# Kernel optimization log

Measured on AMD Instinct MI355X. Metric: run time of the kernel, lower is better.

The kernel has to match this reference:

```python
import jax, jax.numpy as jnp
import numpy as np

SQ, SK, B, H, D = 2048, 2048, 2, 16, 64
LAYER_NUMBER = 1  # coeff for query_key_layer_scaling
MASK_FILL = -10000.0  # attention_mask_func fill value


def setup_inputs() -> dict:
    key = jax.random.key(0)
    kq, kk, kv = jax.random.split(key, 3)
    query_layer = jax.random.normal(kq, (SQ, B, H, D), dtype=jnp.float32)
    key_layer = jax.random.normal(kk, (SK, B, H, D), dtype=jnp.float32)
    value_layer = jax.random.normal(kv, (SK, B, H, D), dtype=jnp.float32)
    attention_mask = jnp.zeros((B, 1, SQ, SK), dtype=bool)  # ignored for causal mask type
    return {
        "query_layer": query_layer,
        "key_layer": key_layer,
        "value_layer": value_layer,
        "attention_mask": attention_mask,
    }


def reference(query_layer, key_layer, value_layer, attention_mask):
    sq, b, h, d = query_layer.shape
    sk = key_layer.shape[0]
    coeff = float(LAYER_NUMBER)
    norm_factor = np.sqrt(d) * coeff  # norm_factor = sqrt(d) * layer_number

    # BMM1: [b,h,sq,sk] scores, scaled by 1/norm_factor
    scores = jnp.einsum("sbhd,tbhd->bhst", query_layer, key_layer) / norm_factor

    # FusedScaleMaskSoftmax: scale by coeff in fp32, causal mask, softmax
    scores = scores.astype(jnp.float32) * coeff
    causal = jnp.triu(jnp.ones((sq, sk), dtype=bool), k=1)  # True above diagonal -> masked
    scores = jnp.where(causal[None, None], MASK_FILL, scores)
    probs = jax.nn.softmax(scores, axis=-1).astype(query_layer.dtype)

    # dropout p=0.0 -> identity

    # BMM2: context [sq,b,h,d] -> [sq,b,h*d]
    context = jnp.einsum("bhst,tbhd->sbhd", probs, value_layer)
    return context.reshape(sq, b, h * d)
```

## Files before the change

kernel.cpp:

```cpp
#include <hip/hip_runtime.h>

typedef short bf16x8 __attribute__((ext_vector_type(8)));
typedef float f32x4 __attribute__((ext_vector_type(4)));
typedef unsigned u32x4 __attribute__((ext_vector_type(4)));
typedef unsigned u32x2 __attribute__((ext_vector_type(2)));
typedef unsigned short ushort_t;

#define RS 2048
#define LDSK 72
#define QSCALE 0.18033688011f
#define BH_STRIDE (2048*64)

static __device__ __forceinline__ unsigned pkbf(float a, float b) {
    union { float f; unsigned u; } ua, ub; ua.f = a; ub.f = b;
    return ((ua.u + 0x8000u) >> 16) | ((ub.u + 0x8000u) & 0xffff0000u);
}

static __device__ __forceinline__ float fexp2(float x) {
#if __has_builtin(__builtin_amdgcn_exp2f)
    return __builtin_amdgcn_exp2f(x);
#else
    return exp2f(x);
#endif
}

__global__ __launch_bounds__(256)
void prep_bf16(const float* __restrict__ K, const float* __restrict__ V,
               ushort_t* __restrict__ Kbf, ushort_t* __restrict__ Vtb)
{
    __shared__ short Tt[64 * LDSK];
    const int kt = blockIdx.x, bh = blockIdx.y;
    const int t = threadIdx.x;

    {
        const int key = t >> 2, cq = (t & 3) * 16;
        const float* kp = K + (size_t)(kt * 64 + key) * RS + bh * 64 + cq;
        f32x4 a0 = *(const f32x4*)kp,     a1 = *(const f32x4*)(kp + 4);
        f32x4 a2 = *(const f32x4*)(kp + 8), a3 = *(const f32x4*)(kp + 12);
        u32x4 w0, w1;
        w0[0] = pkbf(a0[0], a0[1]); w0[1] = pkbf(a0[2], a0[3]);
        w0[2] = pkbf(a1[0], a1[1]); w0[3] = pkbf(a1[2], a1[3]);
        w1[0] = pkbf(a2[0], a2[1]); w1[1] = pkbf(a2[2], a2[3]);
        w1[2] = pkbf(a3[0], a3[1]); w1[3] = pkbf(a3[2], a3[3]);
        ushort_t* kout = Kbf + (size_t)bh * BH_STRIDE + (size_t)(kt * 64 + key) * 64 + cq;
        *(u32x4*)kout = w0;
        *(u32x4*)(kout + 8) = w1;
    }
    {
        const int vkey = (t & 31) * 2, vd = (t >> 5) * 8;
        const float* vp = V + (size_t)(kt * 64 + vkey) * RS + bh * 64 + vd;
        f32x4 b0 = *(const f32x4*)vp,        b1 = *(const f32x4*)(vp + 4);
        f32x4 c0 = *(const f32x4*)(vp + RS), c1 = *(const f32x4*)(vp + RS + 4);
        #pragma unroll
        for (int i = 0; i < 4; ++i) {
            *(unsigned*)&Tt[(vd + i) * LDSK + vkey]     = pkbf(b0[i], c0[i]);
            *(unsigned*)&Tt[(vd + 4 + i) * LDSK + vkey] = pkbf(b1[i], c1[i]);
        }
    }
    __syncthreads();
    {
        const int d = t >> 2, kq = (t & 3) * 16;
        ushort_t* vout = Vtb + (size_t)bh * BH_STRIDE + (size_t)d * RS + kt * 64 + kq;
        u32x4 w0 = *(const u32x4*)&Tt[d * LDSK + kq];
        u32x4 w1 = *(const u32x4*)&Tt[d * LDSK + kq + 8];
        *(u32x4*)vout = w0;
        *(u32x4*)(vout + 8) = w1;
    }
}

__global__ __launch_bounds__(256, 4)
void fa_fwd2(const float* __restrict__ Q, const ushort_t* __restrict__ Kbf,
             const ushort_t* __restrict__ Vtb, float* __restrict__ Out)
{
    __shared__ short Ksh[64 * LDSK];
    __shared__ short Vt[64 * LDSK];
    __shared__ short Psh[4][16 * LDSK];

    const int x = blockIdx.x;
    const int chunk = x >> 8, idx = x & 255;
    const int bh = idx & 31, s = idx >> 5;
    const int qt = (chunk == 0) ? (31 - s) : (chunk == 1) ? (23 - s)
                 : (chunk == 2) ? s : (8 + s);
    const int base = bh * 64;
    const int tid = threadIdx.x;
    const int wave = tid >> 6, lane = tid & 63;
    const int n15 = lane & 15, quad = lane >> 4;
    const int q0 = qt * 64;

    const int r0 = tid >> 3, cc = (tid & 7) * 8;
    const ushort_t* kb = Kbf + (size_t)bh * BH_STRIDE + r0 * 64 + cc;
    const ushort_t* vb = Vtb + (size_t)bh * BH_STRIDE + (size_t)r0 * RS + cc;

    bf16x8 qf[2];
    {
        const float* qp = Q + (size_t)(q0 + wave * 16 + n15) * RS + base + quad * 8;
        #pragma unroll
        for (int ks = 0; ks < 2; ++ks) {
            f32x4 a0 = *(const f32x4*)(qp + ks * 32) * QSCALE;
            f32x4 a1 = *(const f32x4*)(qp + ks * 32 + 4) * QSCALE;
            union { u32x4 u; bf16x8 s; } w;
            w.u[0] = pkbf(a0[0], a0[1]); w.u[1] = pkbf(a0[2], a0[3]);
            w.u[2] = pkbf(a1[0], a1[1]); w.u[3] = pkbf(a1[2], a1[3]);
            qf[ks] = w.s;
        }
    }

    f32x4 O[4];
    #pragma unroll
    for (int i = 0; i < 4; ++i) O[i] = (f32x4){0.f, 0.f, 0.f, 0.f};
    float l = 0.f;

    u32x4 pk0, pk1, pv0, pv1;
    auto prefetch = [&](int kt) {
        const ushort_t* kp = kb + (size_t)kt * 4096;
        pk0 = *(const u32x4*)kp;
        pk1 = *(const u32x4*)(kp + 32 * 64);
        const ushort_t* vp = vb + kt * 64;
        pv0 = *(const u32x4*)vp;
        pv1 = *(const u32x4*)(vp + 32 * RS);
    };
    auto stage = [&]() {
        *(u32x4*)&Ksh[r0 * LDSK + cc] = pk0;
        *(u32x4*)&Ksh[(r0 + 32) * LDSK + cc] = pk1;
        *(u32x4*)&Vt[r0 * LDSK + cc] = pv0;
        *(u32x4*)&Vt[(r0 + 32) * LDSK + cc] = pv1;
    };

    auto compute = [&](int kb_, bool diag) {
        f32x4 S[4];
        #pragma unroll
        for (int mb = 0; mb < 4; ++mb) {
            f32x4 sv = (f32x4){0.f, 0.f, 0.f, 0.f};
            bf16x8 kf0 = *(const bf16x8*)&Ksh[(mb * 16 + n15) * LDSK + quad * 8];
            sv = __builtin_amdgcn_mfma_f32_16x16x32_bf16(kf0, qf[0], sv, 0, 0, 0);
            bf16x8 kf1 = *(const bf16x8*)&Ksh[(mb * 16 + n15) * LDSK + 32 + quad * 8];
            sv = __builtin_amdgcn_mfma_f32_16x16x32_bf16(kf1, qf[1], sv, 0, 0, 0);
            S[mb] = sv;
        }
        if (diag) {
            int q = q0 + wave * 16 + n15;
            #pragma unroll
            for (int mb = 0; mb < 4; ++mb)
                #pragma unroll
                for (int r = 0; r < 4; ++r)
                    if (kb_ + mb * 16 + quad * 4 + r > q) S[mb][r] = -1e30f;
        }
        float rs = 0.f;
        #pragma unroll
        for (int mb = 0; mb < 4; ++mb) {
            float p0 = fexp2(S[mb][0]), p1 = fexp2(S[mb][1]);
            float p2 = fexp2(S[mb][2]), p3 = fexp2(S[mb][3]);
            rs += (p0 + p1) + (p2 + p3);
            u32x2 w; w[0] = pkbf(p0, p1); w[1] = pkbf(p2, p3);
            *(u32x2*)&Psh[wave][n15 * LDSK + mb * 16 + quad * 4] = w;
        }
        rs += __shfl_xor(rs, 16);
        rs += __shfl_xor(rs, 32);
        l += rs;
        bf16x8 pf0 = *(const bf16x8*)&Psh[wave][n15 * LDSK + quad * 8];
        bf16x8 pf1 = *(const bf16x8*)&Psh[wave][n15 * LDSK + 32 + quad * 8];
        #pragma unroll
        for (int db = 0; db < 4; ++db) {
            bf16x8 vf0 = *(const bf16x8*)&Vt[(db * 16 + n15) * LDSK + quad * 8];
            O[db] = __builtin_amdgcn_mfma_f32_16x16x32_bf16(pf0, vf0, O[db], 0, 0, 0);
            bf16x8 vf1 = *(const bf16x8*)&Vt[(db * 16 + n15) * LDSK + 32 + quad * 8];
            O[db] = __builtin_amdgcn_mfma_f32_16x16x32_bf16(pf1, vf1, O[db], 0, 0, 0);
        }
    };

    prefetch(0);
    for (int kt = 0; kt <= qt; ++kt) {
        __syncthreads();
        stage();
        __syncthreads();
        if (kt < qt) prefetch(kt + 1);
        compute(kt * 64, kt == qt);
    }

    #pragma unroll
    for (int r = 0; r < 4; ++r) {
        float inv = 1.0f / __shfl(l, quad * 4 + r);
        size_t row = (size_t)(q0 + wave * 16 + quad * 4 + r) * RS + base;
        #pragma unroll
        for (int db = 0; db < 4; ++db)
            Out[row + db * 16 + n15] = O[db][r] * inv;
    }
}

__global__ __launch_bounds__(256, 3)
void fa_fwd_fb(const float* __restrict__ Q, const float* __restrict__ K,
               const float* __restrict__ V, float* __restrict__ Out)
{
    __shared__ short Ksh[2][64 * LDSK];
    __shared__ short Vt[2][64 * LDSK];
    __shared__ short Psh[4][16 * LDSK];

    const int qt = 31 - blockIdx.y;
    const int bh = blockIdx.x;
    const int base = bh * 64;
    const int tid = threadIdx.x;
    const int wave = tid >> 6, lane = tid & 63;
    const int n15 = lane & 15, quad = lane >> 4;
    const int q0 = qt * 64;
    const int krow = tid >> 2, kcg = (tid & 3) * 16;
    const int vkey = (tid & 31) * 2, vd = (tid >> 5) * 4;

    bf16x8 qf[2];
    {
        const float* qp = Q + (size_t)(q0 + wave * 16 + n15) * RS + base + quad * 8;
        #pragma unroll
        for (int ks = 0; ks < 2; ++ks) {
            f32x4 a0 = *(const f32x4*)(qp + ks * 32) * QSCALE;
            f32x4 a1 = *(const f32x4*)(qp + ks * 32 + 4) * QSCALE;
            union { u32x4 u; bf16x8 s; } w;
            w.u[0] = pkbf(a0[0], a0[1]); w.u[1] = pkbf(a0[2], a0[3]);
            w.u[2] = pkbf(a1[0], a1[1]); w.u[3] = pkbf(a1[2], a1[3]);
            qf[ks] = w.s;
        }
    }
    f32x4 O[4];
    #pragma unroll
    for (int i = 0; i < 4; ++i) O[i] = (f32x4){0.f, 0.f, 0.f, 0.f};
    float l = 0.f;
    f32x4 rk0, rk1, rk2, rk3, rv0, rv1, rv2, rv3;
    auto prefetch = [&](int kt) {
        const int kb = kt * 64;
        const float* kp = K + (size_t)(kb + krow) * RS + base + kcg;
        rk0 = *(const f32x4*)kp;       rk1 = *(const f32x4*)(kp + 4);
        rk2 = *(const f32x4*)(kp + 8); rk3 = *(const f32x4*)(kp + 12);
        const float* vp = V + (size_t)(kb + vkey) * RS + base + vd;
        rv0 = *(const f32x4*)vp;        rv1 = *(const f32x4*)(vp + RS);
        rv2 = *(const f32x4*)(vp + 32); rv3 = *(const f32x4*)(vp + RS + 32);
    };
    auto stage = [&](int buf) {
        u32x4 w0; w0[0] = pkbf(rk0[0], rk0[1]); w0[1] = pkbf(rk0[2], rk0[3]);
                  w0[2] = pkbf(rk1[0], rk1[1]); w0[3] = pkbf(rk1[2], rk1[3]);
        *(u32x4*)&Ksh[buf][krow * LDSK + kcg] = w0;
        u32x4 w1; w1[0] = pkbf(rk2[0], rk2[1]); w1[1] = pkbf(rk2[2], rk2[3]);
                  w1[2] = pkbf(rk3[0], rk3[1]); w1[3] = pkbf(rk3[2], rk3[3]);
        *(u32x4*)&Ksh[buf][krow * LDSK + kcg + 8] = w1;
        #pragma unroll
        for (int i = 0; i < 4; ++i) {
            *(unsigned*)&Vt[buf][(vd + i) * LDSK + vkey] = pkbf(rv0[i], rv1[i]);
            *(unsigned*)&Vt[buf][(vd + 32 + i) * LDSK + vkey] = pkbf(rv2[i], rv3[i]);
        }
    };
    auto compute = [&](int buf, int kb, bool diag) {
        f32x4 S[4];
        #pragma unroll
        for (int mb = 0; mb < 4; ++mb) {
            f32x4 sv = (f32x4){0.f, 0.f, 0.f, 0.f};
            bf16x8 kf0 = *(const bf16x8*)&Ksh[buf][(mb * 16 + n15) * LDSK + quad * 8];
            sv = __builtin_amdgcn_mfma_f32_16x16x32_bf16(kf0, qf[0], sv, 0, 0, 0);
            bf16x8 kf1 = *(const bf16x8*)&Ksh[buf][(mb * 16 + n15) * LDSK + 32 + quad * 8];
            sv = __builtin_amdgcn_mfma_f32_16x16x32_bf16(kf1, qf[1], sv, 0, 0, 0);
            S[mb] = sv;
        }
        if (diag) {
            int q = q0 + wave * 16 + n15;
            #pragma unroll
            for (int mb = 0; mb < 4; ++mb)
                #pragma unroll
                for (int r = 0; r < 4; ++r)
                    if (kb + mb * 16 + quad * 4 + r > q) S[mb][r] = -1e30f;
        }
        float rs = 0.f;
        #pragma unroll
        for (int mb = 0; mb < 4; ++mb) {
            float p0 = fexp2(S[mb][0]), p1 = fexp2(S[mb][1]);
            float p2 = fexp2(S[mb][2]), p3 = fexp2(S[mb][3]);
            rs += (p0 + p1) + (p2 + p3);
            u32x2 w; w[0] = pkbf(p0, p1); w[1] = pkbf(p2, p3);
            *(u32x2*)&Psh[wave][n15 * LDSK + mb * 16 + quad * 4] = w;
        }
        rs += __shfl_xor(rs, 16);
        rs += __shfl_xor(rs, 32);
        l += rs;
        bf16x8 pf0 = *(const bf16x8*)&Psh[wave][n15 * LDSK + quad * 8];
        bf16x8 pf1 = *(const bf16x8*)&Psh[wave][n15 * LDSK + 32 + quad * 8];
        #pragma unroll
        for (int db = 0; db < 4; ++db) {
            bf16x8 vf0 = *(const bf16x8*)&Vt[buf][(db * 16 + n15) * LDSK + quad * 8];
            O[db] = __builtin_amdgcn_mfma_f32_16x16x32_bf16(pf0, vf0, O[db], 0, 0, 0);
            bf16x8 vf1 = *(const bf16x8*)&Vt[buf][(db * 16 + n15) * LDSK + 32 + quad * 8];
            O[db] = __builtin_amdgcn_mfma_f32_16x16x32_bf16(pf1, vf1, O[db], 0, 0, 0);
        }
    };
    prefetch(0);
    stage(0);
    __syncthreads();
    for (int kt = 0; kt <= qt; ++kt) {
        const int cur = kt & 1;
        if (kt < qt) prefetch(kt + 1);
        compute(cur, kt * 64, kt == qt);
        if (kt < qt) stage(1 - cur);
        __syncthreads();
    }
    #pragma unroll
    for (int r = 0; r < 4; ++r) {
        float inv = 1.0f / __shfl(l, quad * 4 + r);
        size_t row = (size_t)(q0 + wave * 16 + quad * 4 + r) * RS + base;
        #pragma unroll
        for (int db = 0; db < 4; ++db)
            Out[row + db * 16 + n15] = O[db][r] * inv;
    }
}

extern "C" void kernel_launch(void* const* d_in, const int* in_sizes, int n_in,
                              void* d_out, int out_size, void* d_ws, size_t ws_size,
                              hipStream_t stream) {
    const float* Q = (const float*)d_in[0];
    const float* K = (const float*)d_in[1];
    const float* V = (const float*)d_in[2];
    float* Out = (float*)d_out;

    if (ws_size >= (size_t)2 * 32 * BH_STRIDE * sizeof(ushort_t)) {
        ushort_t* Kbf = (ushort_t*)d_ws;
        ushort_t* Vtb = Kbf + (size_t)32 * BH_STRIDE;
        prep_bf16<<<dim3(32, 32), dim3(256), 0, stream>>>(K, V, Kbf, Vtb);
        fa_fwd2<<<dim3(1024), dim3(256), 0, stream>>>(Q, Kbf, Vtb, Out);
    } else {
        fa_fwd_fb<<<dim3(32, 32), dim3(256), 0, stream>>>(Q, K, V, Out);
    }
}
```

Measured before the change: 139.0 us.

## Use two-wave blocks with 32 query rows per wave and direct K fragment loads

Restructures the flash-attention kernel from four waves of 16 query rows into two waves of 32 query rows each, launched as 128-thread blocks. Each K and V fragment is now reused across two query groups. K is no longer staged in LDS; each wave reads its K MFMA fragments straight from the bf16 global workspace. This removes the LDS traffic and barrier work for K and doubles register-level reuse. The cost is higher register pressure, lower occupancy from launch_bounds(128,2), and uncoalesced, redundant global K reads across waves.

```diff
diff --git a/kernel.cpp b/kernel.cpp
--- a/kernel.cpp
+++ b/kernel.cpp
@@ -31,11 +31,10 @@
     __shared__ short Tt[64 * LDSK];
     const int kt = blockIdx.x, bh = blockIdx.y;
     const int t = threadIdx.x;
-
     {
         const int key = t >> 2, cq = (t & 3) * 16;
         const float* kp = K + (size_t)(kt * 64 + key) * RS + bh * 64 + cq;
-        f32x4 a0 = *(const f32x4*)kp,     a1 = *(const f32x4*)(kp + 4);
+        f32x4 a0 = *(const f32x4*)kp,       a1 = *(const f32x4*)(kp + 4);
         f32x4 a2 = *(const f32x4*)(kp + 8), a3 = *(const f32x4*)(kp + 12);
         u32x4 w0, w1;
         w0[0] = pkbf(a0[0], a0[1]); w0[1] = pkbf(a0[2], a0[3]);
@@ -68,13 +67,12 @@
     }
 }
 
-__global__ __launch_bounds__(256, 4)
-void fa_fwd2(const float* __restrict__ Q, const ushort_t* __restrict__ Kbf,
+__global__ __launch_bounds__(128, 2)
+void fa_fwd3(const float* __restrict__ Q, const ushort_t* __restrict__ Kbf,
              const ushort_t* __restrict__ Vtb, float* __restrict__ Out)
 {
-    __shared__ short Ksh[64 * LDSK];
     __shared__ short Vt[64 * LDSK];
-    __shared__ short Psh[4][16 * LDSK];
+    __shared__ short Psh[2][32 * LDSK];
 
     const int x = blockIdx.x;
     const int chunk = x >> 8, idx = x & 255;
@@ -86,14 +84,17 @@
     const int wave = tid >> 6, lane = tid & 63;
     const int n15 = lane & 15, quad = lane >> 4;
     const int q0 = qt * 64;
-
-    const int r0 = tid >> 3, cc = (tid & 7) * 8;
-    const ushort_t* kb = Kbf + (size_t)bh * BH_STRIDE + r0 * 64 + cc;
+    const int qw = q0 + wave * 32;
+
+    const ushort_t* Kb = Kbf + (size_t)bh * BH_STRIDE;
+
+    const int r0 = tid >> 2, cc = (tid & 3) * 16;
     const ushort_t* vb = Vtb + (size_t)bh * BH_STRIDE + (size_t)r0 * RS + cc;
 
-    bf16x8 qf[2];
-    {
-        const float* qp = Q + (size_t)(q0 + wave * 16 + n15) * RS + base + quad * 8;
+    bf16x8 qf[2][2];
+    #pragma unroll
+    for (int qg = 0; qg < 2; ++qg) {
+        const float* qp = Q + (size_t)(qw + qg * 16 + n15) * RS + base + quad * 8;
         #pragma unroll
         for (int ks = 0; ks < 2; ++ks) {
             f32x4 a0 = *(const f32x4*)(qp + ks * 32) * QSCALE;
@@ -101,90 +102,112 @@
             union { u32x4 u; bf16x8 s; } w;
             w.u[0] = pkbf(a0[0], a0[1]); w.u[1] = pkbf(a0[2], a0[3]);
             w.u[2] = pkbf(a1[0], a1[1]); w.u[3] = pkbf(a1[2], a1[3]);
-            qf[ks] = w.s;
-        }
-    }
-
-    f32x4 O[4];
-    #pragma unroll
-    for (int i = 0; i < 4; ++i) O[i] = (f32x4){0.f, 0.f, 0.f, 0.f};
-    float l = 0.f;
-
-    u32x4 pk0, pk1, pv0, pv1;
-    auto prefetch = [&](int kt) {
-        const ushort_t* kp = kb + (size_t)kt * 4096;
-        pk0 = *(const u32x4*)kp;
-        pk1 = *(const u32x4*)(kp + 32 * 64);
+            qf[qg][ks] = w.s;
+        }
+    }
+
+    f32x4 O[2][4];
+    #pragma unroll
+    for (int qg = 0; qg < 2; ++qg)
+        #pragma unroll
+        for (int i = 0; i < 4; ++i) O[qg][i] = (f32x4){0.f, 0.f, 0.f, 0.f};
+    float l[2] = {0.f, 0.f};
+
+    u32x4 pv0, pv1, pv2, pv3;
+    auto prefetchV = [&](int kt) {
         const ushort_t* vp = vb + kt * 64;
-        pv0 = *(const u32x4*)vp;
-        pv1 = *(const u32x4*)(vp + 32 * RS);
-    };
-    auto stage = [&]() {
-        *(u32x4*)&Ksh[r0 * LDSK + cc] = pk0;
-        *(u32x4*)&Ksh[(r0 + 32) * LDSK + cc] = pk1;
+        pv0 = *(const u32x4*)vp;             pv1 = *(const u32x4*)(vp + 8);
+        pv2 = *(const u32x4*)(vp + 32 * RS); pv3 = *(const u32x4*)(vp + 32 * RS + 8);
+    };
+    auto stageV = [&]() {
         *(u32x4*)&Vt[r0 * LDSK + cc] = pv0;
-        *(u32x4*)&Vt[(r0 + 32) * LDSK + cc] = pv1;
-    };
-
-    auto compute = [&](int kb_, bool diag) {
-        f32x4 S[4];
+        *(u32x4*)&Vt[r0 * LDSK + cc + 8] = pv1;
+        *(u32x4*)&Vt[(r0 + 32) * LDSK + cc] = pv2;
+        *(u32x4*)&Vt[(r0 + 32) * LDSK + cc + 8] = pv3;
+    };
+
+    auto compute = [&](int kt) {
+        const int kb = kt * 64;
+        const ushort_t* kfp = Kb + (size_t)(kb + n15) * 64 + quad * 8;
+        bf16x8 kf[4][2];
         #pragma unroll
         for (int mb = 0; mb < 4; ++mb) {
-            f32x4 sv = (f32x4){0.f, 0.f, 0.f, 0.f};
-            bf16x8 kf0 = *(const bf16x8*)&Ksh[(mb * 16 + n15) * LDSK + quad * 8];
-            sv = __builtin_amdgcn_mfma_f32_16x16x32_bf16(kf0, qf[0], sv, 0, 0, 0);
-            bf16x8 kf1 = *(const bf16x8*)&Ksh[(mb * 16 + n15) * LDSK + 32 + quad * 8];
-            sv = __builtin_amdgcn_mfma_f32_16x16x32_bf16(kf1, qf[1], sv, 0, 0, 0);
-            S[mb] = sv;
-        }
-        if (diag) {
-            int q = q0 + wave * 16 + n15;
-            #pragma unroll
-            for (int mb = 0; mb < 4; ++mb)
+            kf[mb][0] = *(const bf16x8*)(kfp + mb * 16 * 64);
+            kf[mb][1] = *(const bf16x8*)(kfp + mb * 16 * 64 + 32);
+        }
+        f32x4 S[2][4];
+        #pragma unroll
+        for (int mb = 0; mb < 4; ++mb)
+            #pragma unroll
+            for (int qg = 0; qg < 2; ++qg) {
+                f32x4 sv = (f32x4){0.f, 0.f, 0.f, 0.f};
+                sv = __builtin_amdgcn_mfma_f32_16x16x32_bf16(kf[mb][0], qf[qg][0], sv, 0, 0, 0);
+                sv = __builtin_amdgcn_mfma_f32_16x16x32_bf16(kf[mb][1], qf[qg][1], sv, 0, 0, 0);
+                S[qg][mb] = sv;
+            }
+        if (kt == qt) {
+            #pragma unroll
+            for (int qg = 0; qg < 2; ++qg) {
+                int q = qw + qg * 16 + n15;
                 #pragma unroll
-                for (int r = 0; r < 4; ++r)
-                    if (kb_ + mb * 16 + quad * 4 + r > q) S[mb][r] = -1e30f;
-        }
-        float rs = 0.f;
-        #pragma unroll
-        for (int mb = 0; mb < 4; ++mb) {
-            float p0 = fexp2(S[mb][0]), p1 = fexp2(S[mb][1]);
-            float p2 = fexp2(S[mb][2]), p3 = fexp2(S[mb][3]);
-            rs += (p0 + p1) + (p2 + p3);
-            u32x2 w; w[0] = pkbf(p0, p1); w[1] = pkbf(p2, p3);
-            *(u32x2*)&Psh[wave][n15 * LDSK + mb * 16 + quad * 4] = w;
-        }
-        rs += __shfl_xor(rs, 16);
-        rs += __shfl_xor(rs, 32);
-        l += rs;
-        bf16x8 pf0 = *(const bf16x8*)&Psh[wave][n15 * LDSK + quad * 8];
-        bf16x8 pf1 = *(const bf16x8*)&Psh[wave][n15 * LDSK + 32 + quad * 8];
+                for (int mb = 0; mb < 4; ++mb)
+                    #pragma unroll
+                    for (int r = 0; r < 4; ++r)
+                        if (kb + mb * 16 + quad * 4 + r > q) S[qg][mb][r] = -1e30f;
+            }
+        }
+        #pragma unroll
+        for (int qg = 0; qg < 2; ++qg) {
+            float rs = 0.f;
+            #pragma unroll
+            for (int mb = 0; mb < 4; ++mb) {
+                float p0 = fexp2(S[qg][mb][0]), p1 = fexp2(S[qg][mb][1]);
+                float p2 = fexp2(S[qg][mb][2]), p3 = fexp2(S[qg][mb][3]);
+                rs += (p0 + p1) + (p2 + p3);
+                u32x2 w; w[0] = pkbf(p0, p1); w[1] = pkbf(p2, p3);
+                *(u32x2*)&Psh[wave][(qg * 16 + n15) * LDSK + mb * 16 + quad * 4] = w;
+            }
+            rs += __shfl_xor(rs, 16);
+            rs += __shfl_xor(rs, 32);
+            l[qg] += rs;
+        }
+        bf16x8 pf[2][2];
+        #pragma unroll
+        for (int qg = 0; qg < 2; ++qg) {
+            pf[qg][0] = *(const bf16x8*)&Psh[wave][(qg * 16 + n15) * LDSK + quad * 8];
+            pf[qg][1] = *(const bf16x8*)&Psh[wave][(qg * 16 + n15) * LDSK + 32 + quad * 8];
+        }
         #pragma unroll
         for (int db = 0; db < 4; ++db) {
             bf16x8 vf0 = *(const bf16x8*)&Vt[(db * 16 + n15) * LDSK + quad * 8];
-            O[db] = __builtin_amdgcn_mfma_f32_16x16x32_bf16(pf0, vf0, O[db], 0, 0, 0);
             bf16x8 vf1 = *(const bf16x8*)&Vt[(db * 16 + n15) * LDSK + 32 + quad * 8];
-            O[db] = __builtin_amdgcn_mfma_f32_16x16x32_bf16(pf1, vf1, O[db], 0, 0, 0);
-        }
-    };
-
-    prefetch(0);
+            #pragma unroll
+            for (int qg = 0; qg < 2; ++qg) {
+                O[qg][db] = __builtin_amdgcn_mfma_f32_16x16x32_bf16(pf[qg][0], vf0, O[qg][db], 0, 0, 0);
+                O[qg][db] = __builtin_amdgcn_mfma_f32_16x16x32_bf16(pf[qg][1], vf1, O[qg][db], 0, 0, 0);
+            }
+        }
+    };
+
+    prefetchV(0);
     for (int kt = 0; kt <= qt; ++kt) {
         __syncthreads();
-        stage();
+        stageV();
         __syncthreads();
-        if (kt < qt) prefetch(kt + 1);
-        compute(kt * 64, kt == qt);
-    }
-
-    #pragma unroll
-    for (int r = 0; r < 4; ++r) {
-        float inv = 1.0f / __shfl(l, quad * 4 + r);
-        size_t row = (size_t)(q0 + wave * 16 + quad * 4 + r) * RS + base;
-        #pragma unroll
-        for (int db = 0; db < 4; ++db)
-            Out[row + db * 16 + n15] = O[db][r] * inv;
-    }
+        if (kt < qt) prefetchV(kt + 1);
+        compute(kt);
+    }
+
+    #pragma unroll
+    for (int qg = 0; qg < 2; ++qg)
+        #pragma unroll
+        for (int r = 0; r < 4; ++r) {
+            float inv = 1.0f / __shfl(l[qg], quad * 4 + r);
+            size_t row = (size_t)(qw + qg * 16 + quad * 4 + r) * RS + base;
+            #pragma unroll
+            for (int db = 0; db < 4; ++db)
+                Out[row + db * 16 + n15] = O[qg][db][r] * inv;
+        }
 }
 
 __global__ __launch_bounds__(256, 3)
@@ -318,7 +341,7 @@
         ushort_t* Kbf = (ushort_t*)d_ws;
         ushort_t* Vtb = Kbf + (size_t)32 * BH_STRIDE;
         prep_bf16<<<dim3(32, 32), dim3(256), 0, stream>>>(K, V, Kbf, Vtb);
-        fa_fwd2<<<dim3(1024), dim3(256), 0, stream>>>(Q, Kbf, Vtb, Out);
+        fa_fwd3<<<dim3(1024), dim3(128), 0, stream>>>(Q, Kbf, Vtb, Out);
     } else {
         fa_fwd_fb<<<dim3(32, 32), dim3(256), 0, stream>>>(Q, K, V, Out);
     }
```

Measured after the change: 158.5 us. 14.0% more time.
